# Performance work log

Measured on AMD Instinct MI355X. Metric: run time of the kernel, lower is better.

The kernel has to match this reference:

```python
import jax, jax.numpy as jnp
import numpy as np

B, N, DIM = 2, 1024, 1024   # seq_len must equal dim (dots contracts q's feature dim with kkt's n_y dim)
HEADS, DIM_HEAD = 16, 64    # heads * dim_head == dim (required by residual + LayerNorm(dim))
SCALE = DIM_HEAD ** -0.5
EPS = 1e-5


def setup_inputs() -> dict:
    key = jax.random.key(0)
    ks = jax.random.split(key, 7)
    w = 1.0 / np.sqrt(DIM)  # kaiming-ish linear init keeps logits sane
    return {
        "x": jax.random.normal(ks[0], (B, N, DIM), dtype=jnp.float32),
        "y": jax.random.normal(ks[1], (B, N, DIM), dtype=jnp.float32),
        "Wq": jax.random.normal(ks[2], (DIM, DIM), dtype=jnp.float32) * w,
        "Wk": jax.random.normal(ks[3], (DIM, HEADS * DIM_HEAD), dtype=jnp.float32) * w,
        "Wv": jax.random.normal(ks[4], (DIM, HEADS * DIM_HEAD), dtype=jnp.float32) * w,
        "gamma": jnp.ones((DIM,), dtype=jnp.float32),
        "beta": jnp.zeros((DIM,), dtype=jnp.float32),
    }


def _layer_norm(z, gamma, beta):
    m = jnp.mean(z, axis=-1, keepdims=True)
    v = jnp.mean(jnp.square(z - m), axis=-1, keepdims=True)
    return (z - m) * jax.lax.rsqrt(v + EPS) * gamma + beta


def reference(x, y, Wq, Wk, Wv, gamma, beta):
    b, n, _ = y.shape
    q = x @ Wq                                                     # (b, n, dim); shared across heads (torch repeats)
    k = (y @ Wk).reshape(b, n, HEADS, DIM_HEAD).transpose(0, 2, 1, 3)  # (b, h, n, dh)
    v = (y @ Wv).reshape(b, n, HEADS, DIM_HEAD).transpose(0, 2, 1, 3)  # (b, h, n, dh)
    kkt = jnp.einsum('bhid,bhjd->bhij', k, k) * SCALE              # (b, h, n, n)
    dots = jnp.einsum('bid,bhjd->bhij', q, kkt) * SCALE            # contract q's dim (== n) with kkt rows
    attn = jax.nn.softmax(dots, axis=-1)
    out = jnp.einsum('bhij,bhjd->bhid', attn, v)                   # (b, h, n, dh)
    out = out.transpose(0, 2, 1, 3).reshape(b, n, HEADS * DIM_HEAD)
    return _layer_norm(out + y, gamma, beta)
```

## Files before the change

kernel.cpp:

```cpp
#include <hip/hip_runtime.h>

#define NB 2
#define NN 1024
#define ND 1024
#define NH 16
#define SCALE2 0.015625f
#define SCL2E 0.022542182f
#define DEFER_THR 11.0f
#define LNEPS 1e-5f
#define BK 32
#define NSPLIT 4
#define JPS (16 / NSPLIT)

typedef _Float16 f16x8 __attribute__((ext_vector_type(8)));
typedef _Float16 f16x4 __attribute__((ext_vector_type(4)));
typedef float f32x4 __attribute__((ext_vector_type(4)));


__device__ inline void gload_lds16(const void* g, void* l) {
    __builtin_amdgcn_global_load_lds(
        (const __attribute__((address_space(1))) void*)g,
        (__attribute__((address_space(3))) void*)l, 16, 0, 0);
}

__device__ inline f32x4 vmax4(f32x4 a, f32x4 b) {
    f32x4 c;
    c[0] = fmaxf(a[0], b[0]); c[1] = fmaxf(a[1], b[1]);
    c[2] = fmaxf(a[2], b[2]); c[3] = fmaxf(a[3], b[3]);
    return c;
}

__global__ __launch_bounds__(256) void prep(const float* __restrict__ x,
                                            const float* __restrict__ y,
                                            const float* __restrict__ Wq,
                                            const float* __restrict__ Wk,
                                            const float* __restrict__ Wv,
                                            _Float16* __restrict__ xh,
                                            _Float16* __restrict__ yh,
                                            _Float16* __restrict__ WqT,
                                            _Float16* __restrict__ WkT,
                                            _Float16* __restrict__ WvT) {
    __shared__ float tile[32][33];
    const int bid = blockIdx.x;
    const int tid = threadIdx.x;
    if (bid < 2048) {
        const float* src = (bid < 1024) ? x : y;
        _Float16* dst = (bid < 1024) ? xh : yh;
        int base = (bid & 1023) * 2048 + tid * 8;
        f32x4 a = *(const f32x4*)&src[base];
        f32x4 c = *(const f32x4*)&src[base + 4];
        *(f16x4*)&dst[base] = __builtin_convertvector(a, f16x4);
        *(f16x4*)&dst[base + 4] = __builtin_convertvector(c, f16x4);
    } else {
        int seg = (bid - 2048) >> 10;
        int t = (bid - 2048) & 1023;
        const float* src = seg == 0 ? Wq : seg == 1 ? Wk : Wv;
        _Float16* dst = seg == 0 ? WqT : seg == 1 ? WkT : WvT;
        int tx = tid & 31, ty = tid >> 5;
        int c0 = (t & 31) * 32, r0 = (t >> 5) * 32;
#pragma unroll
        for (int i = 0; i < 4; ++i)
            tile[ty + 8 * i][tx] = src[(size_t)(r0 + ty + 8 * i) * 1024 + c0 + tx];
        __syncthreads();
#pragma unroll
        for (int i = 0; i < 4; ++i)
            dst[(size_t)(c0 + ty + 8 * i) * 1024 + r0 + tx] = (_Float16)tile[tx][ty + 8 * i];
    }
}

template <int BM, int BN>
__device__ __forceinline__ void gemm_body(const _Float16* __restrict__ A,
                                          const _Float16* __restrict__ BT,
                                          int lda, int ldb,
                                          int brow, int bcol, int K,
                                          int mode, _Float16* __restrict__ out0,
                                          _Float16* __restrict__ out1,
                                          int ldc, int zoff) {
    __shared__ _Float16 Asm[2][BM * BK];
    __shared__ _Float16 Bsm[2][BN * BK];
    constexpr int MR = BM / 32;
    constexpr int NC = BN / 32;
    constexpr int ABYTES = BM * BK * 2;
    constexpr int NLOAD = (BM + BN) * BK * 2 / 4096;
    static_assert(ABYTES % 4096 == 0, "A region must align to load passes");

    const int tid = threadIdx.x;
    const int lane = tid & 63;
    const int w = tid >> 6;
    const int wr = w >> 1, wc = w & 1;
    const int g = lane >> 4, r = lane & 15;

    f32x4 acc[MR][NC];
#pragma unroll
    for (int m = 0; m < MR; ++m)
#pragma unroll
        for (int n = 0; n < NC; ++n) acc[m][n] = (f32x4){0.f, 0.f, 0.f, 0.f};

    auto stage = [&](int buf, int kof) {
#pragma unroll
        for (int itl = 0; itl < NLOAD; ++itl) {
            int o = itl * 4096 + tid * 16;
            if (o < ABYTES) {
                int row = o >> 6, cb = o & 63;
                gload_lds16((const char*)(A + (size_t)(brow + row) * lda + kof) + cb,
                            (char*)Asm[buf] + o);
            } else {
                int o2 = o - ABYTES;
                int row = o2 >> 6, cb = o2 & 63;
                gload_lds16((const char*)(BT + (size_t)(bcol + row) * ldb + kof) + cb,
                            (char*)Bsm[buf] + o2);
            }
        }
    };

    stage(0, 0);
    __syncthreads();

    int cur = 0;
    const int nk = K / BK;
    for (int kt = 0; kt < nk; ++kt) {
        if (kt + 1 < nk) stage(cur ^ 1, (kt + 1) * BK);
        f16x8 af[MR], bf[NC];
#pragma unroll
        for (int m = 0; m < MR; ++m)
            af[m] = *(const f16x8*)&Asm[cur][((BM / 2) * wr + 16 * m + r) * BK + 8 * g];
#pragma unroll
        for (int n = 0; n < NC; ++n)
            bf[n] = *(const f16x8*)&Bsm[cur][((BN / 2) * wc + 16 * n + r) * BK + 8 * g];
#pragma unroll
        for (int m = 0; m < MR; ++m)
#pragma unroll
            for (int n = 0; n < NC; ++n)
                acc[m][n] = __builtin_amdgcn_mfma_f32_16x16x32_f16(af[m], bf[n], acc[m][n], 0, 0, 0);
        __syncthreads();
        cur ^= 1;
    }

#pragma unroll
    for (int m = 0; m < MR; ++m)
#pragma unroll
        for (int n = 0; n < NC; ++n) {
            const int colg = bcol + (BN / 2) * wc + 16 * n + r;
            const int rowbase = brow + (BM / 2) * wr + 16 * m + 4 * g;
            if (mode == 0) {
#pragma unroll
                for (int r4 = 0; r4 < 4; ++r4)
                    out0[(size_t)(rowbase + r4) * ldc + colg] = (_Float16)acc[m][n][r4];
            } else if (mode == 1) {
                f16x4 pk = __builtin_convertvector(acc[m][n], f16x4);
                *(f16x4*)&out1[(size_t)colg * 2048 + rowbase] = pk;
                int hh = colg >> 6, dh = colg & 63;
#pragma unroll
                for (int r4 = 0; r4 < 4; ++r4) {
                    int kv = rowbase + r4;
                    int bb = kv >> 10, kvl = kv & 1023;
                    size_t flat = (((size_t)((bb * 16 + hh) * 64 + (kvl >> 4)) * 2 + (dh >> 5)) << 9)
                                  + (((kvl & 15) * 4 + ((dh >> 3) & 3)) << 3) + (dh & 7);
                    out0[flat] = pk[r4];
                }
            } else if (mode == 3) {
                int hh = rowbase >> 6, mpart_ = (rowbase >> 4) & 3;
                int bb = colg >> 10, kvl = colg & 1023;
#pragma unroll
                for (int r4 = 0; r4 < 4; ++r4) {
                    int dsub = (rowbase & 63) + r4;
                    size_t flat = (((size_t)((((bb * 16 + hh) * 4 + mpart_) * 16 + (kvl >> 6)) * 2
                                             + ((kvl >> 5) & 1))) << 9)
                                  + (((dsub & 15) * 4 + ((kvl >> 3) & 3)) << 3) + (kvl & 7);
                    out0[flat] = (_Float16)acc[m][n][r4];
                }
            } else {
                int hh = colg >> 6, dh = colg & 63;
#pragma unroll
                for (int r4 = 0; r4 < 4; ++r4) {
                    int row = rowbase + r4;
                    size_t flat = (((size_t)((zoff * 16 + hh) * 64 + (row >> 4)) * 2 + (dh >> 5)) << 9)
                                  + (((row & 15) * 4 + ((dh >> 3) & 3)) << 3) + (dh & 7);
                    out0[flat] = (_Float16)(acc[m][n][r4] * SCL2E);
                }
            }
        }
}

__global__ __launch_bounds__(256) void gemm_a(const _Float16* __restrict__ xh,
                                              const _Float16* __restrict__ yh,
                                              const _Float16* __restrict__ WqT,
                                              const _Float16* __restrict__ WkT,
                                              _Float16* __restrict__ qh,
                                              _Float16* __restrict__ kfrag,
                                              _Float16* __restrict__ kT) {
    const int bid = blockIdx.x;
    const int t = bid & 255;
    if (bid < 256)
        gemm_body<128, 64>(xh, WqT, 1024, 1024, (t >> 4) * 128, (t & 15) * 64, 1024,
                           0, qh, nullptr, 1024, 0);
    else
        gemm_body<128, 64>(yh, WkT, 1024, 1024, (t >> 4) * 128, (t & 15) * 64, 1024,
                           1, kfrag, kT, 0, 0);
}

__global__ __launch_bounds__(256) void gemm_b(const _Float16* __restrict__ qh,
                                              const _Float16* __restrict__ kT,
                                              const _Float16* __restrict__ yh,
                                              const _Float16* __restrict__ WvT,
                                              _Float16* __restrict__ qfrag,
                                              _Float16* __restrict__ vfrag) {
    const int bid = blockIdx.x;
    if (bid < 256) {
        int z = bid >> 7, t = bid & 127;
        gemm_body<128, 64>(qh + (size_t)z * NN * ND, kT + z * NN, 1024, 2048,
                           (t >> 4) * 128, (t & 15) * 64, 1024, 4, qfrag, nullptr, 0, z);
    } else {
        int t = bid - 256;
        gemm_body<128, 64>(WvT, yh, 1024, 1024, (t >> 5) * 128, (t & 31) * 64, 1024,
                           3, vfrag, nullptr, 0, 0);
    }
}

__global__ __launch_bounds__(256) void flash_part(const _Float16* __restrict__ Qfrag,
                                                  const _Float16* __restrict__ Kfrag,
                                                  const _Float16* __restrict__ Vfrag,
                                                  _Float16* __restrict__ opart,
                                                  float* __restrict__ mpart,
                                                  float* __restrict__ lpart) {
    __shared__ _Float16 Ps[4][2][16][72];
    const int it = blockIdx.x;
    const int bh = blockIdx.y;
    const int sp = blockIdx.z;
    const int b = bh >> 4, h = bh & 15;

    const int tid = threadIdx.x;
    const int lane = tid & 63;
    const int w = tid >> 6;
    const int g = lane >> 4, r = lane & 15;
    const int ch8 = ((r << 2) + g) << 3;

    const _Float16* Kf = Kfrag + ((size_t)bh << 16);
    const _Float16* Vf = Vfrag + ((size_t)bh << 16);

    f16x8 qa[2][2];
#pragma unroll
    for (int u = 0; u < 2; ++u)
#pragma unroll
        for (int kk = 0; kk < 2; ++kk)
            qa[u][kk] = *(const f16x8*)
                &Qfrag[((((size_t)bh * 64 + it * 8 + w * 2 + u) * 2 + kk) << 9) + ch8];

    float m_i[2] = {-1e30f, -1e30f}, l_i[2] = {0.f, 0.f};
    f32x4 o[2][4];
#pragma unroll
    for (int u = 0; u < 2; ++u)
#pragma unroll
        for (int n = 0; n < 4; ++n) o[u][n] = (f32x4){0.f, 0.f, 0.f, 0.f};

    for (int jt = sp * JPS; jt < sp * JPS + JPS; ++jt) {
        f16x8 kfr[4][2];
#pragma unroll
        for (int f = 0; f < 4; ++f)
#pragma unroll
            for (int kk = 0; kk < 2; ++kk)
                kfr[f][kk] = *(const f16x8*)&Kf[(jt * 4 + f) * 1024 + kk * 512 + ch8];

        f32x4 sT[2][4];
#pragma unroll
        for (int u = 0; u < 2; ++u)
#pragma unroll
            for (int f = 0; f < 4; ++f) sT[u][f] = (f32x4){0.f, 0.f, 0.f, 0.f};
#pragma unroll
        for (int f = 0; f < 4; ++f)
#pragma unroll
            for (int kk = 0; kk < 2; ++kk)
#pragma unroll
                for (int u = 0; u < 2; ++u)
                    sT[u][f] = __builtin_amdgcn_mfma_f32_16x16x32_f16(kfr[f][kk], qa[u][kk], sT[u][f], 0, 0, 0);

        f16x8 vfr[4][2];
#pragma unroll
        for (int n = 0; n < 4; ++n)
#pragma unroll
            for (int kk = 0; kk < 2; ++kk)
                vfr[n][kk] = *(const f16x8*)&Vf[(n * 16 + jt) * 1024 + kk * 512 + ch8];

#pragma unroll
        for (int u = 0; u < 2; ++u) {
            f32x4 mm = vmax4(vmax4(sT[u][0], sT[u][1]), vmax4(sT[u][2], sT[u][3]));
            float mx = fmaxf(fmaxf(mm[0], mm[1]), fmaxf(mm[2], mm[3]));
            mx = fmaxf(mx, __shfl_xor(mx, 16));
            mx = fmaxf(mx, __shfl_xor(mx, 32));
            if (!__all(mx <= m_i[u] + DEFER_THR)) {
                float mnew = fmaxf(m_i[u], mx);
                float corr = exp2f(m_i[u] - mnew);
                m_i[u] = mnew;
                l_i[u] *= corr;
#pragma unroll
                for (int n = 0; n < 4; ++n) o[u][n] *= corr;
            }
            f32x4 p[4];
#pragma unroll
            for (int f = 0; f < 4; ++f)
#pragma unroll
                for (int reg = 0; reg < 4; ++reg)
                    p[f][reg] = exp2f(sT[u][f][reg] - m_i[u]);
            f32x4 ps4 = (p[0] + p[1]) + (p[2] + p[3]);
            float rs = (ps4[0] + ps4[1]) + (ps4[2] + ps4[3]);
            rs += __shfl_xor(rs, 16);
            rs += __shfl_xor(rs, 32);
            l_i[u] += rs;
#pragma unroll
            for (int f = 0; f < 4; ++f)
                *(f16x4*)&Ps[w][u][r][16 * f + 4 * g] = __builtin_convertvector(p[f], f16x4);
        }

        f16x8 pa[2][2];
#pragma unroll
        for (int u = 0; u < 2; ++u)
#pragma unroll
            for (int kk = 0; kk < 2; ++kk)
                pa[u][kk] = *(const f16x8*)&Ps[w][u][r][kk * 32 + 8 * g];

#pragma unroll
        for (int n = 0; n < 4; ++n)
#pragma unroll
            for (int kk = 0; kk < 2; ++kk)
#pragma unroll
                for (int u = 0; u < 2; ++u)
                    o[u][n] = __builtin_amdgcn_mfma_f32_16x16x32_f16(vfr[n][kk], pa[u][kk], o[u][n], 0, 0, 0);
    }

    _Float16* Ob = opart + (size_t)sp * NB * NN * ND
                   + ((size_t)b * NN + it * 128 + 32 * w) * ND + h * 64;
#pragma unroll
    for (int u = 0; u < 2; ++u) {
        float inv = 1.0f / l_i[u];
#pragma unroll
        for (int n = 0; n < 4; ++n)
            *(f16x4*)&Ob[(size_t)(u * 16 + r) * ND + 16 * n + 4 * g] =
                __builtin_convertvector(o[u][n] * inv, f16x4);
    }
    if (lane < 16) {
        int base = (((sp * NB) + b) * NH + h) * NN + it * 128 + 32 * w + r;
        mpart[base] = m_i[0];
        lpart[base] = l_i[0];
        mpart[base + 16] = m_i[1];
        lpart[base + 16] = l_i[1];
    }
}

__global__ __launch_bounds__(256) void ln_combine(const _Float16* __restrict__ opart,
                                                  const float* __restrict__ mpart,
                                                  const float* __restrict__ lpart,
                                                  const float* __restrict__ Y,
                                                  const float* __restrict__ gamma,
                                                  const float* __restrict__ beta,
                                                  float* __restrict__ Out) {
    const int row = blockIdx.x;
    const int b = row >> 10, n = row & 1023;
    const int t = threadIdx.x;
    const int c0 = t * 4;
    const int h = c0 >> 6;

    float ms[NSPLIT], ls[NSPLIT];
    float M = -1e30f;
#pragma unroll
    for (int s = 0; s < NSPLIT; ++s) {
        int idx = (((s * NB) + b) * NH + h) * NN + n;
        ms[s] = mpart[idx];
        ls[s] = lpart[idx];
        M = fmaxf(M, ms[s]);
    }
    float wsum = 0.f;
    f32x4 acc = (f32x4){0.f, 0.f, 0.f, 0.f};
#pragma unroll
    for (int s = 0; s < NSPLIT; ++s) {
        float wgt = exp2f(ms[s] - M) * ls[s];
        wsum += wgt;
        f16x4 ov = *(const f16x4*)&opart[(size_t)s * NB * NN * ND + (size_t)row * ND + c0];
        acc += wgt * __builtin_convertvector(ov, f32x4);
    }
    f32x4 z = acc * (1.0f / wsum) + *(const f32x4*)&Y[(size_t)row * ND + c0];

    __shared__ float red[8];
    float s1 = z.x + z.y + z.z + z.w;
#pragma unroll
    for (int off = 32; off; off >>= 1) s1 += __shfl_xor(s1, off);
    if ((t & 63) == 0) red[t >> 6] = s1;
    __syncthreads();
    float mean = (red[0] + red[1] + red[2] + red[3]) * (1.0f / 1024.0f);

    f32x4 d = z - mean;
    float sq = d.x * d.x + d.y * d.y + d.z * d.z + d.w * d.w;
#pragma unroll
    for (int off = 32; off; off >>= 1) sq += __shfl_xor(sq, off);
    if ((t & 63) == 0) red[4 + (t >> 6)] = sq;
    __syncthreads();
    float var = (red[4] + red[5] + red[6] + red[7]) * (1.0f / 1024.0f);
    float rstd = rsqrtf(var + LNEPS);

    f32x4 gg = *(const f32x4*)&gamma[c0];
    f32x4 bb = *(const f32x4*)&beta[c0];
    f32x4 res = d * rstd * gg + bb;
    *(f32x4*)&Out[(size_t)row * ND + c0] = res;
}

extern "C" void kernel_launch(void* const* d_in, const int* in_sizes, int n_in,
                              void* d_out, int out_size, void* d_ws, size_t ws_size,
                              hipStream_t stream) {
    const float* x = (const float*)d_in[0];
    const float* y = (const float*)d_in[1];
    const float* Wq = (const float*)d_in[2];
    const float* Wk = (const float*)d_in[3];
    const float* Wv = (const float*)d_in[4];
    const float* gamma = (const float*)d_in[5];
    const float* beta = (const float*)d_in[6];
    float* out = (float*)d_out;

    const size_t MB = 1024ull * 1024ull;
    char* w = (char*)d_ws;
    _Float16* xh    = (_Float16*)(w + 0 * MB);
    _Float16* yh    = (_Float16*)(w + 4 * MB);
    _Float16* WqT   = (_Float16*)(w + 8 * MB);
    _Float16* WkT   = (_Float16*)(w + 10 * MB);
    _Float16* WvT   = (_Float16*)(w + 12 * MB);
    _Float16* qh    = (_Float16*)(w + 14 * MB);
    _Float16* kT    = (_Float16*)(w + 18 * MB);
    _Float16* kfrag = (_Float16*)(w + 22 * MB);
    _Float16* vfrag = (_Float16*)(w + 26 * MB);
    _Float16* qfrag = (_Float16*)(w + 30 * MB);
    _Float16* opart = (_Float16*)(w + 34 * MB);
    float* mpart = (float*)(w + 50 * MB);
    float* lpart = (float*)(w + 50 * MB + 512 * 1024);

    prep<<<5120, 256, 0, stream>>>(x, y, Wq, Wk, Wv, xh, yh, WqT, WkT, WvT);

    gemm_a<<<512, 256, 0, stream>>>(xh, yh, WqT, WkT, qh, kfrag, kT);

    gemm_b<<<512, 256, 0, stream>>>(qh, kT, yh, WvT, qfrag, vfrag);

    flash_part<<<dim3(8, 32, NSPLIT), 256, 0, stream>>>(qfrag, kfrag, vfrag, opart, mpart, lpart);

    ln_combine<<<NB * NN, 256, 0, stream>>>(opart, mpart, lpart, y, gamma, beta, out);
}
```

Baseline: 92.06 us.

## Double-buffer K/V tiles in LDS via async global loads and halve KV split

The flash attention kernel now stages each K and V tile into double-buffered shared memory with global_load_lds, prefetching the next tile while the current one is computed, instead of each wave reading K/V fragments straight from global memory. The KV split count drops from 4 to 2, so each block processes twice as many tiles and the combine kernel reads fewer partials. The aim is to hide global load latency and remove redundant per-wave global reads of shared K/V. The cost is a barrier per iteration, extra LDS use, and half as many blocks in flight.

```diff
diff --git a/kernel.cpp b/kernel.cpp
--- a/kernel.cpp
+++ b/kernel.cpp
@@ -9,7 +9,7 @@
 #define DEFER_THR 11.0f
 #define LNEPS 1e-5f
 #define BK 32
-#define NSPLIT 4
+#define NSPLIT 2
 #define JPS (16 / NSPLIT)
 
 typedef _Float16 f16x8 __attribute__((ext_vector_type(8)));
@@ -223,6 +223,8 @@
                                                   _Float16* __restrict__ opart,
                                                   float* __restrict__ mpart,
                                                   float* __restrict__ lpart) {
+    __shared__ _Float16 Ks[2][4096];
+    __shared__ _Float16 Vs[2][4096];
     __shared__ _Float16 Ps[4][2][16][72];
     const int it = blockIdx.x;
     const int bh = blockIdx.y;
@@ -238,6 +240,21 @@
     const _Float16* Kf = Kfrag + ((size_t)bh << 16);
     const _Float16* Vf = Vfrag + ((size_t)bh << 16);
 
+    auto stageKV = [&](int buf, int jt) {
+#pragma unroll
+        for (int q = 0; q < 2; ++q) {
+            int c = q * 4 + w;
+            gload_lds16(&Kf[jt * 4096 + c * 512 + lane * 8], &Ks[buf][c * 512 + lane * 8]);
+        }
+#pragma unroll
+        for (int q = 0; q < 2; ++q) {
+            int c = q * 4 + w;
+            int n = c >> 1, half = c & 1;
+            gload_lds16(&Vf[(n * 16 + jt) * 1024 + half * 512 + lane * 8],
+                        &Vs[buf][n * 1024 + half * 512 + lane * 8]);
+        }
+    };
+
     f16x8 qa[2][2];
 #pragma unroll
     for (int u = 0; u < 2; ++u)
@@ -253,13 +270,20 @@
 #pragma unroll
         for (int n = 0; n < 4; ++n) o[u][n] = (f32x4){0.f, 0.f, 0.f, 0.f};
 
-    for (int jt = sp * JPS; jt < sp * JPS + JPS; ++jt) {
+    const int jt0 = sp * JPS;
+    stageKV(0, jt0);
+    __syncthreads();
+
+    int buf = 0;
+    for (int j = 0; j < JPS; ++j) {
+        if (j + 1 < JPS) stageKV(buf ^ 1, jt0 + j + 1);
+
         f16x8 kfr[4][2];
 #pragma unroll
         for (int f = 0; f < 4; ++f)
 #pragma unroll
             for (int kk = 0; kk < 2; ++kk)
-                kfr[f][kk] = *(const f16x8*)&Kf[(jt * 4 + f) * 1024 + kk * 512 + ch8];
+                kfr[f][kk] = *(const f16x8*)&Ks[buf][(f * 2 + kk) * 512 + ch8];
 
         f32x4 sT[2][4];
 #pragma unroll
@@ -279,7 +303,7 @@
         for (int n = 0; n < 4; ++n)
 #pragma unroll
             for (int kk = 0; kk < 2; ++kk)
-                vfr[n][kk] = *(const f16x8*)&Vf[(n * 16 + jt) * 1024 + kk * 512 + ch8];
+                vfr[n][kk] = *(const f16x8*)&Vs[buf][n * 1024 + kk * 512 + ch8];
 
 #pragma unroll
         for (int u = 0; u < 2; ++u) {
@@ -325,6 +349,9 @@
 #pragma unroll
                 for (int u = 0; u < 2; ++u)
                     o[u][n] = __builtin_amdgcn_mfma_f32_16x16x32_f16(vfr[n][kk], pa[u][kk], o[u][n], 0, 0, 0);
+
+        __syncthreads();
+        buf ^= 1;
     }
 
     _Float16* Ob = opart + (size_t)sp * NB * NN * ND
@@ -427,8 +454,8 @@
     _Float16* vfrag = (_Float16*)(w + 26 * MB);
     _Float16* qfrag = (_Float16*)(w + 30 * MB);
     _Float16* opart = (_Float16*)(w + 34 * MB);
-    float* mpart = (float*)(w + 50 * MB);
-    float* lpart = (float*)(w + 50 * MB + 512 * 1024);
+    float* mpart = (float*)(w + 42 * MB);
+    float* lpart = (float*)(w + 43 * MB);
 
     prep<<<5120, 256, 0, stream>>>(x, y, Wq, Wk, Wv, xh, yh, WqT, WkT, WvT);
 
```

Measured after the change: 90.29 us. About the same (-1.9%).
